# Kernel optimization log

Hardware: AMD Instinct MI355X
Metric: run time of the kernel (lower is better)

The kernel has to match this reference:

```python
import jax, jax.numpy as jnp
import numpy as np
from jax import lax

LSTM_UNITS = 64
BATCH = 2048
TIMESTEPS = 1024


def _lstm_cell(x, h, c, W_ih, W_hh, b_ih, b_hh):
    # PyTorch LSTMCell gate order: i, f, g, o
    gates = x @ W_ih.T + b_ih + h @ W_hh.T + b_hh
    i, f, g, o = jnp.split(gates, 4, axis=-1)
    c_new = jax.nn.sigmoid(f) * c + jax.nn.sigmoid(i) * jnp.tanh(g)
    h_new = jax.nn.sigmoid(o) * jnp.tanh(c_new)
    return h_new, c_new


def setup_inputs() -> dict:
    key = jax.random.key(0)
    ks = jax.random.split(key, 9)
    U = LSTM_UNITS
    s0 = 1.0 / np.sqrt(U)  # torch LSTMCell init scale (hidden=64)
    s1 = 1.0  # hidden=1 -> scale 1/sqrt(1)
    inp = {
        "input": jax.random.normal(ks[0], (BATCH, TIMESTEPS), dtype=jnp.float32),
        # c0: LSTMCell(1, 64)
        "W_ih0": jax.random.uniform(ks[1], (4 * U, 1), jnp.float32, -s0, s0),
        "W_hh0": jax.random.uniform(ks[2], (4 * U, U), jnp.float32, -s0, s0),
        "b_ih0": jax.random.uniform(ks[3], (4 * U,), jnp.float32, -s0, s0),
        "b_hh0": jax.random.uniform(ks[4], (4 * U,), jnp.float32, -s0, s0),
        # c1: LSTMCell(64, 1)
        "W_ih1": jax.random.uniform(ks[5], (4, U), jnp.float32, -s1, s1),
        "W_hh1": jax.random.uniform(ks[6], (4, 1), jnp.float32, -s1, s1),
        "b_ih1": jax.random.uniform(ks[7], (4,), jnp.float32, -s1, s1),
        "b_hh1": jax.random.uniform(ks[8], (4,), jnp.float32, -s1, s1),
    }
    return inp


def reference(input, W_ih0, W_hh0, b_ih0, b_hh0, W_ih1, W_hh1, b_ih1, b_hh1):
    B = input.shape[0]
    U = LSTM_UNITS
    dt = input.dtype
    h0 = jnp.zeros((B, U), dt)
    c0 = jnp.zeros((B, U), dt)
    h1 = jnp.zeros((B, 1), dt)
    c1 = jnp.zeros((B, 1), dt)

    def step(carry, x_t):
        h0, c0, h1, c1 = carry
        h0n, c0n = _lstm_cell(x_t, h0, c0, W_ih0, W_hh0, b_ih0, b_hh0)
        # NOTE: the original feeds the CELL state c0n (not h0n) into layer 2
        h1n, c1n = _lstm_cell(c0n, h1, c1, W_ih1, W_hh1, b_ih1, b_hh1)
        # output per step is the cell state of layer 2
        return (h0n, c0n, h1n, c1n), c1n

    xs = input.T[:, :, None]  # (T, B, 1)
    _, ys = lax.scan(step, (h0, c0, h1, c1), xs)  # ys: (T, B, 1)
    return ys[:, :, 0].T  # (B, T)
```

## Files before the change

### kernel.cpp

```cpp
#include <hip/hip_runtime.h>

#define T_STEPS 1024
#define BATCH 2048
#define BTILE 4
#define HS 36

typedef short short8 __attribute__((ext_vector_type(8)));
typedef float f32x4 __attribute__((ext_vector_type(4)));
typedef float f32x2 __attribute__((ext_vector_type(2)));

__device__ __forceinline__ float fast_rcp(float x) {
#if __has_builtin(__builtin_amdgcn_rcpf)
    return __builtin_amdgcn_rcpf(x);
#else
    return 1.0f / x;
#endif
}

__device__ __forceinline__ float fast_exp2(float x) {
#if __has_builtin(__builtin_amdgcn_exp2f)
    return __builtin_amdgcn_exp2f(x);
#else
    return exp2f(x);
#endif
}

__device__ __forceinline__ float sigf(float x) {
    return fast_rcp(1.0f + fast_exp2(-1.44269504f * x));
}

__device__ __forceinline__ f32x2 sigf2(f32x2 v) {
    f32x2 t = v * (-1.44269504f);
    f32x2 e = {fast_exp2(t[0]), fast_exp2(t[1])};
    e = e + 1.0f;
    return f32x2{fast_rcp(e[0]), fast_rcp(e[1])};
}

__device__ __forceinline__ float tanh_fast(float x) {
    float e = fast_exp2(2.88539008f * x);
    return 1.0f - 2.0f * fast_rcp(e + 1.0f);
}

__device__ __forceinline__ unsigned f2bf(float x) {
    unsigned u = __float_as_uint(x);
    unsigned r = u + 0x7FFFu + ((u >> 16) & 1u);
    return r >> 16;
}
__device__ __forceinline__ float bf2f(unsigned b) {
    return __uint_as_float(b << 16);
}

__device__ __forceinline__ unsigned cvt_pk_bf16(float a, float b) {
    unsigned r;
    asm("v_cvt_pk_bf16_f32 %0, %1, %2" : "=v"(r) : "v"(a), "v"(b));
    return r;
}

__device__ __forceinline__ float sel4A(f32x4 a) {
    int v = __float_as_int(a[0]);
    v = __builtin_amdgcn_update_dpp(v, __float_as_int(a[1]), 0x114, 0xf, 0x2, false);
    v = __builtin_amdgcn_update_dpp(v, __float_as_int(a[2]), 0x118, 0xf, 0x4, false);
    v = __builtin_amdgcn_update_dpp(v, __float_as_int(a[3]), 0x11C, 0xf, 0x8, false);
    return __int_as_float(v);
}
__device__ __forceinline__ float dpp_shl4f(float v) {
    return __int_as_float(__builtin_amdgcn_update_dpp(0, __float_as_int(v), 0x104, 0xf, 0xf, true));
}

__device__ __forceinline__ void step_barrier() {
    asm volatile("s_waitcnt lgkmcnt(0)" ::: "memory");
    __builtin_amdgcn_s_barrier();
    asm volatile("" ::: "memory");
}

__device__ __forceinline__ f32x4 l2_mfma(short8 ch0, short8 ch1,
                                         short8 cl0, short8 cl1,
                                         const short8* a2h, const short8* a2l) {
    f32x4 zA = {0.0f, 0.0f, 0.0f, 0.0f};
    f32x4 zB = {0.0f, 0.0f, 0.0f, 0.0f};
    zA = __builtin_amdgcn_mfma_f32_16x16x32_bf16(a2h[0], ch0, zA, 0, 0, 0);
    zB = __builtin_amdgcn_mfma_f32_16x16x32_bf16(a2l[1], ch1, zB, 0, 0, 0);
    zA = __builtin_amdgcn_mfma_f32_16x16x32_bf16(a2h[1], ch1, zA, 0, 0, 0);
    zB = __builtin_amdgcn_mfma_f32_16x16x32_bf16(a2h[0], cl0, zB, 0, 0, 0);
    zA = __builtin_amdgcn_mfma_f32_16x16x32_bf16(a2l[0], ch0, zA, 0, 0, 0);
    zB = __builtin_amdgcn_mfma_f32_16x16x32_bf16(a2h[1], cl1, zB, 0, 0, 0);
    return zA + zB;
}

__device__ __forceinline__ void l2_act(f32x4 z2, float& h1r, float& c1r,
                                       const float* whh1v, const float* b1v,
                                       int l, float* __restrict__ out,
                                       int bb, int tout, bool upd) {
    float g1i = z2[0] + b1v[0] + h1r * whh1v[0];
    float g1f = z2[1] + b1v[1] + h1r * whh1v[1];
    float g1g = z2[2] + b1v[2] + h1r * whh1v[2];
    float g1o = z2[3] + b1v[3] + h1r * whh1v[3];
    float c1n = sigf(g1f) * c1r + sigf(g1i) * tanh_fast(g1g);
    float h1n = sigf(g1o) * tanh_fast(c1n);
    if (l < 4) {
        out[(size_t)(bb + l) * T_STEPS + tout] = c1n;
        if (upd) { h1r = h1n; c1r = c1n; }
    }
}

__global__ __launch_bounds__(256, 2)
void lstm_v12_kernel(const float* __restrict__ input,
                     const float* __restrict__ W_ih0,
                     const float* __restrict__ W_hh0,
                     const float* __restrict__ b_ih0,
                     const float* __restrict__ b_hh0,
                     const float* __restrict__ W_ih1,
                     const float* __restrict__ W_hh1,
                     const float* __restrict__ b_ih1,
                     const float* __restrict__ b_hh1,
                     float* __restrict__ out)
{
    const int tid = threadIdx.x;
    const int w   = tid >> 6;
    const int l   = tid & 63;
    const int q16 = l >> 4;
    const int n16 = l & 15;
    const int nb  = l & 3;
    const int r   = (l >> 2) & 3;
    const int u   = 16 * w + 4 * q16 + r;
    const int bbase = blockIdx.x * BTILE;

    __shared__ __align__(16) unsigned Hbuf[2][3][16][HS];
    __shared__ float Xb[2][BTILE][65];

    for (int i = tid; i < 2 * 3 * 16 * HS; i += 256)
        reinterpret_cast<unsigned*>(Hbuf)[i] = 0u;

    short8 a1[4][2];
    #pragma unroll
    for (int g = 0; g < 4; ++g) {
        #pragma unroll
        for (int kt = 0; kt < 2; ++kt) {
            const float* p = W_hh0 + (size_t)(16 * (w + 4 * g) + n16) * 64 + kt * 32 + q16 * 8;
            short8 a;
            #pragma unroll
            for (int j = 0; j < 8; ++j) a[j] = (short)f2bf(p[j]);
            a1[g][kt] = a;
        }
    }
    short8 a2h[2], a2l[2];
    #pragma unroll
    for (int kt = 0; kt < 2; ++kt) {
        short8 ah = {0,0,0,0,0,0,0,0}, al = {0,0,0,0,0,0,0,0};
        if (n16 < 4) {
            const float* p = W_ih1 + (size_t)n16 * 64 + kt * 32 + q16 * 8;
            #pragma unroll
            for (int j = 0; j < 8; ++j) {
                unsigned hb = f2bf(p[j]);
                ah[j] = (short)hb;
                al[j] = (short)f2bf(p[j] - bf2f(hb));
            }
        }
        a2h[kt] = ah; a2l[kt] = al;
    }

    f32x2 w01, w23, b01, b23;
    {
        float wgv[4], bgv[4];
        #pragma unroll
        for (int g = 0; g < 4; ++g) {
            int row = g * 64 + u;
            wgv[g] = W_ih0[row];
            bgv[g] = b_ih0[row] + b_hh0[row];
        }
        w01 = f32x2{wgv[0], wgv[1]}; w23 = f32x2{wgv[2], wgv[3]};
        b01 = f32x2{bgv[0], bgv[1]}; b23 = f32x2{bgv[2], bgv[3]};
    }
    float whh1v[4], b1v[4];
    #pragma unroll
    for (int g = 0; g < 4; ++g) { whh1v[g] = W_hh1[g]; b1v[g] = b_ih1[g] + b_hh1[g]; }

    const float* inrow = input + (size_t)(bbase + w) * T_STEPS;
    Xb[0][w][l] = inrow[l];
    float xnext = 0.0f;
    float c0 = 0.0f;

    short8 r_ch0 = {0,0,0,0,0,0,0,0}, r_ch1 = {0,0,0,0,0,0,0,0};
    short8 r_cl0 = {0,0,0,0,0,0,0,0}, r_cl1 = {0,0,0,0,0,0,0,0};
    float h1r = 0.0f, c1r = 0.0f;

    __syncthreads();

    if (blockIdx.x & 256) {
        __builtin_amdgcn_s_sleep(5);
    }

    int par = 0;
    #pragma unroll 2
    for (int t = 0; t < T_STEPS; ++t) {
        if ((t & 63) == 0 && t + 64 < T_STEPS) xnext = inrow[t + 64 + l];
        const int cp = (t >> 6) & 1;

        const unsigned* Hrow = &Hbuf[par][0][n16][0];
        short8 hb0 = *reinterpret_cast<const short8*>(Hrow + 4 * q16);
        short8 hb1 = *reinterpret_cast<const short8*>(Hrow + 16 + 4 * q16);

        f32x4 z2 = {0.0f, 0.0f, 0.0f, 0.0f};
        const bool do2 = (w == 3) && (t >= 2);
        if (do2)
            z2 = l2_mfma(r_ch0, r_ch1, r_cl0, r_cl1, a2h, a2l);

        if (w == 3 && t >= 1) {
            const unsigned* Ch = &Hbuf[par][1][n16][0];
            const unsigned* Cl = &Hbuf[par][2][n16][0];
            r_ch0 = *reinterpret_cast<const short8*>(Ch + 4 * q16);
            r_ch1 = *reinterpret_cast<const short8*>(Ch + 16 + 4 * q16);
            r_cl0 = *reinterpret_cast<const short8*>(Cl + 4 * q16);
            r_cl1 = *reinterpret_cast<const short8*>(Cl + 16 + 4 * q16);
        }

        f32x4 accv[4];
        #pragma unroll
        for (int g = 0; g < 4; ++g) {
            f32x4 z = {0.0f, 0.0f, 0.0f, 0.0f};
            z = __builtin_amdgcn_mfma_f32_16x16x32_bf16(a1[g][0], hb0, z, 0, 0, 0);
            z = __builtin_amdgcn_mfma_f32_16x16x32_bf16(a1[g][1], hb1, z, 0, 0, 0);
            accv[g] = z;
        }

        if (do2)
            l2_act(z2, h1r, c1r, whh1v, b1v, l, out, bbase, t - 2, true);

        float g4[4];
        #pragma unroll
        for (int g = 0; g < 4; ++g) g4[g] = sel4A(accv[g]);

        float x = Xb[cp][nb][t & 63];
        f32x2 xx = {x, x};
        f32x2 gif = f32x2{g4[0], g4[1]} + (xx * w01 + b01);
        f32x2 ggo = f32x2{g4[2], g4[3]} + (xx * w23 + b23);

        f32x2 sif = sigf2(gif);
        float tg  = tanh_fast(ggo[0]);
        float c0n = sif[1] * c0 + sif[0] * tg;
        c0 = c0n;
        float h0n = sigf(ggo[1]) * tanh_fast(c0n);

        float ph = dpp_shl4f(h0n);
        float pc = dpp_shl4f(c0n);
        unsigned hword  = cvt_pk_bf16(h0n, ph);
        unsigned chword = cvt_pk_bf16(c0n, pc);
        float hi_own = bf2f(chword & 0xFFFFu);
        float lo_own = c0n - hi_own;
        float plo = dpp_shl4f(lo_own);
        unsigned clword = cvt_pk_bf16(lo_own, plo);
        if (!(l & 4)) {
            int widx = 8 * w + 2 * q16 + (r >> 1);
            Hbuf[par ^ 1][0][nb][widx] = hword;
            Hbuf[par ^ 1][1][nb][widx] = chword;
            Hbuf[par ^ 1][2][nb][widx] = clword;
        }
        if ((t & 63) == 63 && t + 1 < T_STEPS) Xb[cp ^ 1][w][l] = xnext;

        step_barrier();
        par ^= 1;
    }

    if (w == 3) {
        f32x4 z2 = l2_mfma(r_ch0, r_ch1, r_cl0, r_cl1, a2h, a2l);
        l2_act(z2, h1r, c1r, whh1v, b1v, l, out, bbase, T_STEPS - 2, true);
        const unsigned* Ch = &Hbuf[par][1][n16][0];
        const unsigned* Cl = &Hbuf[par][2][n16][0];
        short8 ch0 = *reinterpret_cast<const short8*>(Ch + 4 * q16);
        short8 ch1 = *reinterpret_cast<const short8*>(Ch + 16 + 4 * q16);
        short8 cl0 = *reinterpret_cast<const short8*>(Cl + 4 * q16);
        short8 cl1 = *reinterpret_cast<const short8*>(Cl + 16 + 4 * q16);
        f32x4 z3 = l2_mfma(ch0, ch1, cl0, cl1, a2h, a2l);
        l2_act(z3, h1r, c1r, whh1v, b1v, l, out, bbase, T_STEPS - 1, false);
    }
}

extern "C" void kernel_launch(void* const* d_in, const int* in_sizes, int n_in,
                              void* d_out, int out_size, void* d_ws, size_t ws_size,
                              hipStream_t stream) {
    const float* input = (const float*)d_in[0];
    const float* W_ih0 = (const float*)d_in[1];
    const float* W_hh0 = (const float*)d_in[2];
    const float* b_ih0 = (const float*)d_in[3];
    const float* b_hh0 = (const float*)d_in[4];
    const float* W_ih1 = (const float*)d_in[5];
    const float* W_hh1 = (const float*)d_in[6];
    const float* b_ih1 = (const float*)d_in[7];
    const float* b_hh1 = (const float*)d_in[8];
    float* out = (float*)d_out;

    dim3 grid(BATCH / BTILE);
    dim3 block(256);
    lstm_v12_kernel<<<grid, block, 0, stream>>>(
        input, W_ih0, W_hh0, b_ih0, b_hh0, W_ih1, W_hh1, b_ih1, b_hh1, out);
}
```

Before: 588.4 us.

## Make each wave own full recurrence for two batch rows, removing block barriers

Restructures the kernel so each wavefront computes all 64 hidden units for two batch rows, with per-wave LDS ping-pong buffers, eliminating the per-step block barrier. Layer-2 work is fused into every wave's step, one step behind. The cost is 16 row-tile MFMA pairs per wave per step with only 2 of 16 batch columns used, doubling total matrix work, and launch bounds drop to one block per SIMD group.

```diff
diff --git a/kernel.cpp b/kernel.cpp
--- a/kernel.cpp
+++ b/kernel.cpp
@@ -2,8 +2,7 @@
 
 #define T_STEPS 1024
 #define BATCH 2048
-#define BTILE 4
-#define HS 36
+#define PS 36
 
 typedef short short8 __attribute__((ext_vector_type(8)));
 typedef float f32x4 __attribute__((ext_vector_type(4)));
@@ -16,7 +15,6 @@
     return 1.0f / x;
 #endif
 }
-
 __device__ __forceinline__ float fast_exp2(float x) {
 #if __has_builtin(__builtin_amdgcn_exp2f)
     return __builtin_amdgcn_exp2f(x);
@@ -24,23 +22,19 @@
     return exp2f(x);
 #endif
 }
-
 __device__ __forceinline__ float sigf(float x) {
     return fast_rcp(1.0f + fast_exp2(-1.44269504f * x));
 }
-
 __device__ __forceinline__ f32x2 sigf2(f32x2 v) {
     f32x2 t = v * (-1.44269504f);
     f32x2 e = {fast_exp2(t[0]), fast_exp2(t[1])};
     e = e + 1.0f;
     return f32x2{fast_rcp(e[0]), fast_rcp(e[1])};
 }
-
 __device__ __forceinline__ float tanh_fast(float x) {
     float e = fast_exp2(2.88539008f * x);
     return 1.0f - 2.0f * fast_rcp(e + 1.0f);
 }
-
 __device__ __forceinline__ unsigned f2bf(float x) {
     unsigned u = __float_as_uint(x);
     unsigned r = u + 0x7FFFu + ((u >> 16) & 1u);
@@ -49,33 +43,40 @@
 __device__ __forceinline__ float bf2f(unsigned b) {
     return __uint_as_float(b << 16);
 }
-
 __device__ __forceinline__ unsigned cvt_pk_bf16(float a, float b) {
     unsigned r;
     asm("v_cvt_pk_bf16_f32 %0, %1, %2" : "=v"(r) : "v"(a), "v"(b));
     return r;
 }
 
-__device__ __forceinline__ float sel4A(f32x4 a) {
-    int v = __float_as_int(a[0]);
-    v = __builtin_amdgcn_update_dpp(v, __float_as_int(a[1]), 0x114, 0xf, 0x2, false);
-    v = __builtin_amdgcn_update_dpp(v, __float_as_int(a[2]), 0x118, 0xf, 0x4, false);
-    v = __builtin_amdgcn_update_dpp(v, __float_as_int(a[3]), 0x11C, 0xf, 0x8, false);
+__device__ __forceinline__ float sel_merge(f32x4 A, f32x4 C) {
+    int v = __float_as_int(A[0]);
+    v = __builtin_amdgcn_update_dpp(v, __float_as_int(A[1]), 0x114, 0xf, 0x2, false);
+    v = __builtin_amdgcn_update_dpp(v, __float_as_int(A[2]), 0x118, 0xf, 0x4, false);
+    v = __builtin_amdgcn_update_dpp(v, __float_as_int(A[3]), 0x11C, 0xf, 0x8, false);
+    v = __builtin_amdgcn_update_dpp(v, __float_as_int(C[0]), 0x112, 0xf, 0x1, false);
+    v = __builtin_amdgcn_update_dpp(v, __float_as_int(C[1]), 0x116, 0xf, 0x2, false);
+    v = __builtin_amdgcn_update_dpp(v, __float_as_int(C[2]), 0x11A, 0xf, 0x4, false);
+    v = __builtin_amdgcn_update_dpp(v, __float_as_int(C[3]), 0x11E, 0xf, 0x8, false);
     return __int_as_float(v);
 }
 __device__ __forceinline__ float dpp_shl4f(float v) {
     return __int_as_float(__builtin_amdgcn_update_dpp(0, __float_as_int(v), 0x104, 0xf, 0xf, true));
 }
 
-__device__ __forceinline__ void step_barrier() {
-    asm volatile("s_waitcnt lgkmcnt(0)" ::: "memory");
-    __builtin_amdgcn_s_barrier();
-    asm volatile("" ::: "memory");
-}
-
-__device__ __forceinline__ f32x4 l2_mfma(short8 ch0, short8 ch1,
-                                         short8 cl0, short8 cl1,
-                                         const short8* a2h, const short8* a2l) {
+__device__ __forceinline__ void l2_step(const unsigned* br, int fro,
+                                        const short8* a2h, const short8* a2l,
+                                        const float* whh1v, const float* b1v,
+                                        float& h1r, float& c1r,
+                                        int l, float* __restrict__ out,
+                                        int bb, int tout)
+{
+    const unsigned* Ch = br + 2 * PS;
+    const unsigned* Cl = br + 4 * PS;
+    short8 ch0 = *reinterpret_cast<const short8*>(Ch + fro);
+    short8 ch1 = *reinterpret_cast<const short8*>(Ch + fro + 16);
+    short8 cl0 = *reinterpret_cast<const short8*>(Cl + fro);
+    short8 cl1 = *reinterpret_cast<const short8*>(Cl + fro + 16);
     f32x4 zA = {0.0f, 0.0f, 0.0f, 0.0f};
     f32x4 zB = {0.0f, 0.0f, 0.0f, 0.0f};
     zA = __builtin_amdgcn_mfma_f32_16x16x32_bf16(a2h[0], ch0, zA, 0, 0, 0);
@@ -84,27 +85,21 @@
     zB = __builtin_amdgcn_mfma_f32_16x16x32_bf16(a2h[0], cl0, zB, 0, 0, 0);
     zA = __builtin_amdgcn_mfma_f32_16x16x32_bf16(a2l[0], ch0, zA, 0, 0, 0);
     zB = __builtin_amdgcn_mfma_f32_16x16x32_bf16(a2h[1], cl1, zB, 0, 0, 0);
-    return zA + zB;
-}
-
-__device__ __forceinline__ void l2_act(f32x4 z2, float& h1r, float& c1r,
-                                       const float* whh1v, const float* b1v,
-                                       int l, float* __restrict__ out,
-                                       int bb, int tout, bool upd) {
-    float g1i = z2[0] + b1v[0] + h1r * whh1v[0];
-    float g1f = z2[1] + b1v[1] + h1r * whh1v[1];
-    float g1g = z2[2] + b1v[2] + h1r * whh1v[2];
-    float g1o = z2[3] + b1v[3] + h1r * whh1v[3];
+    f32x4 z = zA + zB;
+    float g1i = z[0] + b1v[0] + h1r * whh1v[0];
+    float g1f = z[1] + b1v[1] + h1r * whh1v[1];
+    float g1g = z[2] + b1v[2] + h1r * whh1v[2];
+    float g1o = z[3] + b1v[3] + h1r * whh1v[3];
     float c1n = sigf(g1f) * c1r + sigf(g1i) * tanh_fast(g1g);
     float h1n = sigf(g1o) * tanh_fast(c1n);
-    if (l < 4) {
+    if (l < 2)
         out[(size_t)(bb + l) * T_STEPS + tout] = c1n;
-        if (upd) { h1r = h1n; c1r = c1n; }
-    }
-}
-
-__global__ __launch_bounds__(256, 2)
-void lstm_v12_kernel(const float* __restrict__ input,
+    h1r = h1n;
+    c1r = c1n;
+}
+
+__global__ __launch_bounds__(256, 1)
+void lstm_v15_kernel(const float* __restrict__ input,
                      const float* __restrict__ W_ih0,
                      const float* __restrict__ W_hh0,
                      const float* __restrict__ b_ih0,
@@ -120,27 +115,29 @@
     const int l   = tid & 63;
     const int q16 = l >> 4;
     const int n16 = l & 15;
-    const int nb  = l & 3;
+    const int c   = l & 3;
+    const int nb  = c & 1;
+    const int uh  = c >> 1;
     const int r   = (l >> 2) & 3;
-    const int u   = 16 * w + 4 * q16 + r;
-    const int bbase = blockIdx.x * BTILE;
-
-    __shared__ __align__(16) unsigned Hbuf[2][3][16][HS];
-    __shared__ float Xb[2][BTILE][65];
-
-    for (int i = tid; i < 2 * 3 * 16 * HS; i += 256)
-        reinterpret_cast<unsigned*>(Hbuf)[i] = 0u;
-
-    short8 a1[4][2];
-    #pragma unroll
-    for (int g = 0; g < 4; ++g) {
+    const int rh  = (l >> 3) & 1;
+    const int bb  = blockIdx.x * 8 + w * 2;
+
+    __shared__ __align__(16) unsigned HP[4][2][3][2][PS];
+    __shared__ float Xb[4][2][2][65];
+
+    for (int i = l; i < 2 * 3 * 2 * PS; i += 64)
+        reinterpret_cast<unsigned*>(HP[w])[i] = 0u;
+
+    short8 a1[16][2];
+    #pragma unroll
+    for (int rt = 0; rt < 16; ++rt) {
         #pragma unroll
         for (int kt = 0; kt < 2; ++kt) {
-            const float* p = W_hh0 + (size_t)(16 * (w + 4 * g) + n16) * 64 + kt * 32 + q16 * 8;
+            const float* p = W_hh0 + (size_t)(16 * rt + n16) * 64 + kt * 32 + q16 * 8;
             short8 a;
             #pragma unroll
             for (int j = 0; j < 8; ++j) a[j] = (short)f2bf(p[j]);
-            a1[g][kt] = a;
+            a1[rt][kt] = a;
         }
     }
     short8 a2h[2], a2l[2];
@@ -159,120 +156,104 @@
         a2h[kt] = ah; a2l[kt] = al;
     }
 
-    f32x2 w01, w23, b01, b23;
-    {
+    f32x2 w01[2], w23[2], b01[2], b23[2];
+    #pragma unroll
+    for (int jj = 0; jj < 2; ++jj) {
+        const int u = 32 * jj + 16 * uh + 4 * q16 + r;
         float wgv[4], bgv[4];
         #pragma unroll
-        for (int g = 0; g < 4; ++g) {
-            int row = g * 64 + u;
-            wgv[g] = W_ih0[row];
-            bgv[g] = b_ih0[row] + b_hh0[row];
-        }
-        w01 = f32x2{wgv[0], wgv[1]}; w23 = f32x2{wgv[2], wgv[3]};
-        b01 = f32x2{bgv[0], bgv[1]}; b23 = f32x2{bgv[2], bgv[3]};
+        for (int gg = 0; gg < 4; ++gg) {
+            int row = gg * 64 + u;
+            wgv[gg] = W_ih0[row];
+            bgv[gg] = b_ih0[row] + b_hh0[row];
+        }
+        w01[jj] = f32x2{wgv[0], wgv[1]}; w23[jj] = f32x2{wgv[2], wgv[3]};
+        b01[jj] = f32x2{bgv[0], bgv[1]}; b23[jj] = f32x2{bgv[2], bgv[3]};
     }
     float whh1v[4], b1v[4];
     #pragma unroll
     for (int g = 0; g < 4; ++g) { whh1v[g] = W_hh1[g]; b1v[g] = b_ih1[g] + b_hh1[g]; }
 
-    const float* inrow = input + (size_t)(bbase + w) * T_STEPS;
-    Xb[0][w][l] = inrow[l];
-    float xnext = 0.0f;
-    float c0 = 0.0f;
-
-    short8 r_ch0 = {0,0,0,0,0,0,0,0}, r_ch1 = {0,0,0,0,0,0,0,0};
-    short8 r_cl0 = {0,0,0,0,0,0,0,0}, r_cl1 = {0,0,0,0,0,0,0,0};
+    const float* inrowA = input + (size_t)bb * T_STEPS;
+    const float* inrowB = inrowA + T_STEPS;
+    Xb[w][0][0][l] = inrowA[l];
+    Xb[w][0][1][l] = inrowB[l];
+    float xnA = 0.0f, xnB = 0.0f;
+    float c0s[2] = {0.0f, 0.0f};
     float h1r = 0.0f, c1r = 0.0f;
 
-    __syncthreads();
-
-    if (blockIdx.x & 256) {
-        __builtin_amdgcn_s_sleep(5);
-    }
-
+    const int fro = nb * PS + 4 * q16;
     int par = 0;
-    #pragma unroll 2
+
     for (int t = 0; t < T_STEPS; ++t) {
-        if ((t & 63) == 0 && t + 64 < T_STEPS) xnext = inrow[t + 64 + l];
+        if ((t & 63) == 0 && t + 64 < T_STEPS) {
+            xnA = inrowA[t + 64 + l];
+            xnB = inrowB[t + 64 + l];
+        }
         const int cp = (t >> 6) & 1;
 
-        const unsigned* Hrow = &Hbuf[par][0][n16][0];
-        short8 hb0 = *reinterpret_cast<const short8*>(Hrow + 4 * q16);
-        short8 hb1 = *reinterpret_cast<const short8*>(Hrow + 16 + 4 * q16);
-
-        f32x4 z2 = {0.0f, 0.0f, 0.0f, 0.0f};
-        const bool do2 = (w == 3) && (t >= 2);
-        if (do2)
-            z2 = l2_mfma(r_ch0, r_ch1, r_cl0, r_cl1, a2h, a2l);
-
-        if (w == 3 && t >= 1) {
-            const unsigned* Ch = &Hbuf[par][1][n16][0];
-            const unsigned* Cl = &Hbuf[par][2][n16][0];
-            r_ch0 = *reinterpret_cast<const short8*>(Ch + 4 * q16);
-            r_ch1 = *reinterpret_cast<const short8*>(Ch + 16 + 4 * q16);
-            r_cl0 = *reinterpret_cast<const short8*>(Cl + 4 * q16);
-            r_cl1 = *reinterpret_cast<const short8*>(Cl + 16 + 4 * q16);
-        }
-
-        f32x4 accv[4];
-        #pragma unroll
-        for (int g = 0; g < 4; ++g) {
+        const unsigned* br = &HP[w][par][0][0][0];
+        unsigned*       bw = &HP[w][par ^ 1][0][0][0];
+
+        short8 hb0 = *reinterpret_cast<const short8*>(br + fro);
+        short8 hb1 = *reinterpret_cast<const short8*>(br + fro + 16);
+
+        f32x4 acc[16];
+        #pragma unroll
+        for (int rt = 0; rt < 16; ++rt) {
             f32x4 z = {0.0f, 0.0f, 0.0f, 0.0f};
-            z = __builtin_amdgcn_mfma_f32_16x16x32_bf16(a1[g][0], hb0, z, 0, 0, 0);
-            z = __builtin_amdgcn_mfma_f32_16x16x32_bf16(a1[g][1], hb1, z, 0, 0, 0);
-            accv[g] = z;
-        }
-
-        if (do2)
-            l2_act(z2, h1r, c1r, whh1v, b1v, l, out, bbase, t - 2, true);
-
-        float g4[4];
-        #pragma unroll
-        for (int g = 0; g < 4; ++g) g4[g] = sel4A(accv[g]);
-
-        float x = Xb[cp][nb][t & 63];
+            z = __builtin_amdgcn_mfma_f32_16x16x32_bf16(a1[rt][0], hb0, z, 0, 0, 0);
+            z = __builtin_amdgcn_mfma_f32_16x16x32_bf16(a1[rt][1], hb1, z, 0, 0, 0);
+            acc[rt] = z;
+        }
+
+        if (t > 0)
+            l2_step(br, fro, a2h, a2l, whh1v, b1v, h1r, c1r, l, out, bb, t - 1);
+
+        float g4[2][4];
+        #pragma unroll
+        for (int jj = 0; jj < 2; ++jj)
+            #pragma unroll
+            for (int gg = 0; gg < 4; ++gg)
+                g4[jj][gg] = sel_merge(acc[4 * gg + 2 * jj], acc[4 * gg + 2 * jj + 1]);
+
+        float x = Xb[w][cp][nb][t & 63];
         f32x2 xx = {x, x};
-        f32x2 gif = f32x2{g4[0], g4[1]} + (xx * w01 + b01);
-        f32x2 ggo = f32x2{g4[2], g4[3]} + (xx * w23 + b23);
-
-        f32x2 sif = sigf2(gif);
-        float tg  = tanh_fast(ggo[0]);
-        float c0n = sif[1] * c0 + sif[0] * tg;
-        c0 = c0n;
-        float h0n = sigf(ggo[1]) * tanh_fast(c0n);
-
-        float ph = dpp_shl4f(h0n);
-        float pc = dpp_shl4f(c0n);
-        unsigned hword  = cvt_pk_bf16(h0n, ph);
-        unsigned chword = cvt_pk_bf16(c0n, pc);
-        float hi_own = bf2f(chword & 0xFFFFu);
-        float lo_own = c0n - hi_own;
-        float plo = dpp_shl4f(lo_own);
-        unsigned clword = cvt_pk_bf16(lo_own, plo);
-        if (!(l & 4)) {
-            int widx = 8 * w + 2 * q16 + (r >> 1);
-            Hbuf[par ^ 1][0][nb][widx] = hword;
-            Hbuf[par ^ 1][1][nb][widx] = chword;
-            Hbuf[par ^ 1][2][nb][widx] = clword;
-        }
-        if ((t & 63) == 63 && t + 1 < T_STEPS) Xb[cp ^ 1][w][l] = xnext;
-
-        step_barrier();
+        #pragma unroll
+        for (int jj = 0; jj < 2; ++jj) {
+            f32x2 gif = f32x2{g4[jj][0], g4[jj][1]} + (xx * w01[jj] + b01[jj]);
+            f32x2 ggo = f32x2{g4[jj][2], g4[jj][3]} + (xx * w23[jj] + b23[jj]);
+            f32x2 sif = sigf2(gif);
+            float tg  = tanh_fast(ggo[0]);
+            float c0n = sif[1] * c0s[jj] + sif[0] * tg;
+            c0s[jj] = c0n;
+            float h0n = sigf(ggo[1]) * tanh_fast(c0n);
+
+            float ph = dpp_shl4f(h0n);
+            float pc = dpp_shl4f(c0n);
+            unsigned hword  = cvt_pk_bf16(h0n, ph);
+            unsigned chword = cvt_pk_bf16(c0n, pc);
+            float hi_own = bf2f(chword & 0xFFFFu);
+            float lo_own = c0n - hi_own;
+            float plo = dpp_shl4f(lo_own);
+            unsigned clword = cvt_pk_bf16(lo_own, plo);
+            if (!(l & 4)) {
+                int widx = nb * PS + 16 * jj + 8 * uh + 2 * q16 + rh;
+                bw[widx]          = hword;
+                bw[2 * PS + widx] = chword;
+                bw[4 * PS + widx] = clword;
+            }
+        }
+
+        if ((t & 63) == 63 && t + 1 < T_STEPS) {
+            Xb[w][cp ^ 1][0][l] = xnA;
+            Xb[w][cp ^ 1][1][l] = xnB;
+        }
         par ^= 1;
     }
 
-    if (w == 3) {
-        f32x4 z2 = l2_mfma(r_ch0, r_ch1, r_cl0, r_cl1, a2h, a2l);
-        l2_act(z2, h1r, c1r, whh1v, b1v, l, out, bbase, T_STEPS - 2, true);
-        const unsigned* Ch = &Hbuf[par][1][n16][0];
-        const unsigned* Cl = &Hbuf[par][2][n16][0];
-        short8 ch0 = *reinterpret_cast<const short8*>(Ch + 4 * q16);
-        short8 ch1 = *reinterpret_cast<const short8*>(Ch + 16 + 4 * q16);
-        short8 cl0 = *reinterpret_cast<const short8*>(Cl + 4 * q16);
-        short8 cl1 = *reinterpret_cast<const short8*>(Cl + 16 + 4 * q16);
-        f32x4 z3 = l2_mfma(ch0, ch1, cl0, cl1, a2h, a2l);
-        l2_act(z3, h1r, c1r, whh1v, b1v, l, out, bbase, T_STEPS - 1, false);
-    }
+    l2_step(&HP[w][par][0][0][0], fro, a2h, a2l, whh1v, b1v,
+            h1r, c1r, l, out, bb, T_STEPS - 1);
 }
 
 extern "C" void kernel_launch(void* const* d_in, const int* in_sizes, int n_in,
@@ -289,8 +270,8 @@
     const float* b_hh1 = (const float*)d_in[8];
     float* out = (float*)d_out;
 
-    dim3 grid(BATCH / BTILE);
+    dim3 grid(BATCH / 8);
     dim3 block(256);
-    lstm_v12_kernel<<<grid, block, 0, stream>>>(
+    lstm_v15_kernel<<<grid, block, 0, stream>>>(
         input, W_ih0, W_hh0, b_ih0, b_hh0, W_ih1, W_hh1, b_ih1, b_hh1, out);
 }
```

Result: slower. 980.0 us (+66.5%).
